# Performance work log

Measured on AMD Instinct MI355X. Metric: run time of the kernel, lower is better.

Reference implementation:

```python
import jax, jax.numpy as jnp
from jax import lax
import numpy as np
import math

V, D, N, L, KC, KL, B, S = 32000, 1024, 64, 4, 4, 4, 2, 1024
SCALE = 1.0 / math.sqrt(2 * L)   # base_layer.residual_scale
GAMMA = 0.01                     # lindblad_gamma
COND_TH = 100.0                  # condition_threshold
PHASE = np.complex64(np.exp(1j * 0.1))  # quaternionic escape rotation


def setup_inputs() -> dict:
    key = jax.random.key(0)
    ks = jax.random.split(key, 16)
    g = lambda k, shp, s=0.02: jax.random.normal(k, shp, jnp.float32) * s
    return {
        'token_ids': jax.random.randint(ks[0], (B, S), 0, V, dtype=jnp.int32),
        'emb_r': g(ks[1], (V, D)),
        'emb_i': g(ks[2], (V, D)),
        'W_in': g(ks[3], (L, D, 2 * D)),
        'conv_k': g(ks[4], (L, D, KC), 0.2),
        'A_log': jax.random.normal(ks[5], (L, D, N), jnp.float32) * 0.5,
        'dt_scale': g(ks[6], (L, D), 1.0),
        'dt_bias': jnp.full((L, D), -2.0, jnp.float32),
        'W_B': g(ks[7], (L, N, D)),
        'W_C': g(ks[8], (L, N, D)),
        'D_skip': g(ks[9], (L, D), 0.1),
        'W_out': g(ks[10], (L, D, D)),
        'L_ops': g(ks[11], (L, KL, D), 0.1),
        'norm_w': jnp.ones((D,), jnp.float32),
    }


def _dwconv(x, k):
    # causal depthwise conv; x [B,S,D] real, k [D,KC]
    xt = jnp.transpose(x, (0, 2, 1))  # [B,D,S]
    pad = k.shape[-1] - 1
    y = lax.conv_general_dilated(xt, k[:, None, :], (1,), [(pad, 0)],
                                 feature_group_count=k.shape[0])
    return jnp.transpose(y, (0, 2, 1))


def _csilu(x):
    # complex 'silu': x * sigmoid(|x|)
    return x * jax.nn.sigmoid(jnp.abs(x))


def _layer(x, Wi, ck, Alog, dts, dtb, WB, WC, Dk, Wo, Lops):
    residual = x
    xz = jnp.einsum('bsd,de->bse', x, Wi)          # complex [B,S,2D]
    x1, z = xz[..., :D], xz[..., D:]
    x1 = _dwconv(x1.real, ck) + 1j * _dwconv(x1.imag, ck)
    x1 = _csilu(x1)
    dt = jax.nn.softplus(x1.real * dts + dtb)      # [B,S,D] real
    A = -jnp.exp(Alog)                             # [D,N] real, stable
    Bc = jnp.einsum('bsd,nd->bsn', x1, WB)         # complex [B,S,N]
    Cc = jnp.einsum('bsd,nd->bsn', x1, WC)

    def step(h, inp):
        dt_t, x_t, B_t, C_t = inp                  # [B,D],[B,D],[B,N],[B,N]
        decay = jnp.exp(dt_t[..., None] * A)       # [B,D,N] real
        h = decay * h + (dt_t * x_t)[..., None] * B_t[:, None, :]
        y = jnp.einsum('bdn,bn->bd', h, C_t)
        return h, y

    h0 = jnp.zeros((x.shape[0], D, N), jnp.complex64)
    xs = (jnp.transpose(dt, (1, 0, 2)), jnp.transpose(x1, (1, 0, 2)),
          jnp.transpose(Bc, (1, 0, 2)), jnp.transpose(Cc, (1, 0, 2)))
    _, ys = lax.scan(step, h0, xs)                 # [S,B,D]
    y = jnp.transpose(ys, (1, 0, 2)) + Dk * x1
    y = y * _csilu(z)
    branch = jnp.einsum('bsd,de->bse', y, Wo)      # branch_out = (out-res)/scale

    # Lindblad dissipation: psi -> psi - gamma * sum_k L_k (L_k^H psi)
    proj = jnp.einsum('bsd,kd->bsk', branch, Lops)
    branch = branch - GAMMA * jnp.einsum('bsk,kd->bsd', proj, Lops)

    # H_eff = mean_s |psi_s><psi_s|; quaternionic escape uses its conditioning.
    # Only the diagonal is needed for the (diag-approx) condition number.
    diag = jnp.mean(jnp.abs(branch) ** 2, axis=1)  # [B,D]
    cond = jnp.max(diag, -1) / (jnp.min(diag, -1) + 1e-8)
    phase = jnp.where(cond > COND_TH, PHASE, jnp.complex64(1.0))  # [B]
    branch = branch * phase[:, None, None]

    # hybrid automata: _H_prev is None on first forward -> no jump (faithful)
    return residual + SCALE * branch


def reference(token_ids, emb_r, emb_i, W_in, conv_k, A_log, dt_scale, dt_bias,
              W_B, W_C, D_skip, W_out, L_ops, norm_w):
    psi = emb_r[token_ids] + 1j * emb_i[token_ids]   # [B,S,D] complex64
    for l in range(L):
        psi = _layer(psi, W_in[l], conv_k[l], A_log[l], dt_scale[l],
                     dt_bias[l], W_B[l], W_C[l], D_skip[l], W_out[l], L_ops[l])
    # ComplexRMSNorm
    rms = jnp.sqrt(jnp.mean(jnp.abs(psi) ** 2, -1, keepdims=True) + 1e-8)
    psi = psi / rms * norm_w
    # Born collapse sampler with weight tied to real embedding
    amp_r = jnp.einsum('bsd,vd->bsv', psi.real, emb_r)
    amp_i = jnp.einsum('bsd,vd->bsv', psi.imag, emb_r)
    logits = jnp.log(amp_r ** 2 + amp_i ** 2 + 1e-8)  # [B,S,V] real
    return logits
```

## Files before the change

kernel.cpp:

```cpp
#include <hip/hip_runtime.h>
#include <math.h>

#define BB 2
#define SS 1024
#define DD 1024
#define NN 64
#define LLAYERS 4
#define KCC 4
#define KLL 4
#define VV 32000
#define MM (BB*SS)
#define M2 (2*MM)
#define PS ((size_t)MM*DD)
#define CH 4
#define LC (SS/CH)
#define BDW (BB*DD)

#define SCALE_F 0.35355339059327373f
#define GAMMA_F 0.01f
#define PHASE_COS 0.99500416527802576f
#define PHASE_SIN 0.09983341664682815f

typedef _Float16 f16x8 __attribute__((ext_vector_type(8)));
typedef _Float16 f16x4 __attribute__((ext_vector_type(4)));
typedef float f32x4 __attribute__((ext_vector_type(4)));

__device__ __forceinline__ float softplus_f(float x) {
    return fmaxf(x, 0.f) + log1pf(expf(-fabsf(x)));
}

__device__ __forceinline__ void async16(void* lds_dst, const void* g_src) {
    __builtin_amdgcn_global_load_lds(
        (const __attribute__((address_space(1))) unsigned int*)g_src,
        (__attribute__((address_space(3))) unsigned int*)lds_dst,
        16, 0, 0);
}

__device__ __forceinline__ float rsum64_dpp(float v) {
    int x;
    x = __float_as_int(v);
    v += __int_as_float(__builtin_amdgcn_update_dpp(0, x, 0x111, 0xf, 0xf, true));
    x = __float_as_int(v);
    v += __int_as_float(__builtin_amdgcn_update_dpp(0, x, 0x112, 0xf, 0xf, true));
    x = __float_as_int(v);
    v += __int_as_float(__builtin_amdgcn_update_dpp(0, x, 0x114, 0xf, 0xf, true));
    x = __float_as_int(v);
    v += __int_as_float(__builtin_amdgcn_update_dpp(0, x, 0x118, 0xf, 0xf, true));
    x = __float_as_int(v);
    v += __int_as_float(__builtin_amdgcn_update_dpp(0, x, 0x142, 0xa, 0xf, true));
    x = __float_as_int(v);
    v += __int_as_float(__builtin_amdgcn_update_dpp(0, x, 0x143, 0xc, 0xf, true));
    return v;
}

__global__ __launch_bounds__(256) void k_split_w(const float* __restrict__ W,
        _Float16* __restrict__ Wh, _Float16* __restrict__ Wl, int Ksz, int Nsz) {
    __shared__ float t[32][33];
    int k0 = blockIdx.x * 32, n0 = blockIdx.y * 32;
    size_t base = (size_t)blockIdx.z * Ksz * Nsz;
    int r = threadIdx.x >> 3, c4 = (threadIdx.x & 7) * 4;
    float4 v = *(const float4*)(W + base + (size_t)(k0 + r) * Nsz + n0 + c4);
    t[r][c4 + 0] = v.x; t[r][c4 + 1] = v.y; t[r][c4 + 2] = v.z; t[r][c4 + 3] = v.w;
    __syncthreads();
    f16x4 hi, lo;
    #pragma unroll
    for (int j = 0; j < 4; ++j) {
        float x = t[c4 + j][r];
        _Float16 h = (_Float16)x;
        hi[j] = h; lo[j] = (_Float16)(x - (float)h);
    }
    size_t o = base + (size_t)(n0 + r) * Ksz + k0 + c4;
    *(f16x4*)(Wh + o) = hi;
    *(f16x4*)(Wl + o) = lo;
}

__global__ __launch_bounds__(256) void k_embed(const int* __restrict__ tok,
        const float* __restrict__ er, const float* __restrict__ ei,
        float* __restrict__ Pr, float* __restrict__ Pi,
        _Float16* __restrict__ Ph, _Float16* __restrict__ Pl) {
    int i = blockIdx.x * 256 + threadIdx.x;
    int d4 = (i & (DD/4 - 1)) * 4;
    int m  = i >> 8;
    int t = tok[m];
    float4 r  = *(const float4*)(er + (size_t)t * DD + d4);
    float4 im = *(const float4*)(ei + (size_t)t * DD + d4);
    size_t o = (size_t)m * DD + d4;
    *(float4*)(Pr + o) = r;
    *(float4*)(Pi + o) = im;
    float vr[4] = {r.x, r.y, r.z, r.w}, vi[4] = {im.x, im.y, im.z, im.w};
    f16x4 rh, rl, ih, il;
    #pragma unroll
    for (int j = 0; j < 4; ++j) {
        _Float16 h = (_Float16)vr[j]; rh[j] = h; rl[j] = (_Float16)(vr[j] - (float)h);
        _Float16 g = (_Float16)vi[j]; ih[j] = g; il[j] = (_Float16)(vi[j] - (float)g);
    }
    *(f16x4*)(Ph + o) = rh;      *(f16x4*)(Pl + o) = rl;
    *(f16x4*)(Ph + PS + o) = ih; *(f16x4*)(Pl + PS + o) = il;
}

__global__ __launch_bounds__(256, 2) void k_gemm_f16(
        const _Float16* __restrict__ Ah, const _Float16* __restrict__ Al,
        const _Float16* __restrict__ Bh, const _Float16* __restrict__ Bl,
        float* __restrict__ C, int Nsz) {
    __shared__ __align__(16) unsigned char lds[32768];
    const int lane = threadIdx.x & 63;
    const int wid  = threadIdx.x >> 6;
    const int wm = (wid >> 1) * 64;
    const int wv = (wid & 1) * 64;
    const int n0 = blockIdx.x * 128;
    const int m0 = blockIdx.y * 128;
    const int fr = lane & 15, fq = lane >> 4;

    f32x4 acc[4][4] = {};

    for (int k0 = 0; k0 < 1024; k0 += 32) {
        #pragma unroll
        for (int j = 0; j < 8; ++j) {
            int cid = wid * 8 + j;
            int sel = cid >> 3, c = cid & 7;
            const _Float16* bp = (sel == 0) ? Ah : (sel == 1) ? Al : (sel == 2) ? Bh : Bl;
            int rbase = ((sel < 2) ? m0 : n0) + c * 16 + fr;
            async16(lds + cid * 1024, bp + (size_t)rbase * 1024 + k0 + fq * 8);
        }
        __syncthreads();

        f16x8 ah[4], al[4];
        #pragma unroll
        for (int ms = 0; ms < 4; ++ms) {
            int off = ((wm >> 4) + ms) * 1024 + lane * 16;
            ah[ms] = *(const f16x8*)(lds + off);
            al[ms] = *(const f16x8*)(lds + 8192 + off);
        }
        #pragma unroll
        for (int vs = 0; vs < 4; ++vs) {
            int boff = ((wv >> 4) + vs) * 1024 + lane * 16;
            f16x8 bh = *(const f16x8*)(lds + 16384 + boff);
            f16x8 bl = *(const f16x8*)(lds + 24576 + boff);
            #pragma unroll
            for (int ms = 0; ms < 4; ++ms) {
                acc[ms][vs] = __builtin_amdgcn_mfma_f32_16x16x32_f16(ah[ms], bh, acc[ms][vs], 0, 0, 0);
                acc[ms][vs] = __builtin_amdgcn_mfma_f32_16x16x32_f16(ah[ms], bl, acc[ms][vs], 0, 0, 0);
                acc[ms][vs] = __builtin_amdgcn_mfma_f32_16x16x32_f16(al[ms], bh, acc[ms][vs], 0, 0, 0);
            }
        }
        __syncthreads();
    }

    #pragma unroll
    for (int ms = 0; ms < 4; ++ms) {
        #pragma unroll
        for (int vs = 0; vs < 4; ++vs) {
            #pragma unroll
            for (int r = 0; r < 4; ++r) {
                int row = m0 + wm + ms * 16 + fq * 4 + r;
                int col = n0 + wv + vs * 16 + fr;
                C[(size_t)row * Nsz + col] = acc[ms][vs][r];
            }
        }
    }
}

__global__ __launch_bounds__(256) void k_conv(const float* __restrict__ XZ,
        const float* __restrict__ ck, const float* __restrict__ dts,
        const float* __restrict__ dtb,
        float* __restrict__ Xr, float* __restrict__ Xi, float* __restrict__ DT,
        float* __restrict__ ZUr, float* __restrict__ ZUi) {
    int i = blockIdx.x * 256 + threadIdx.x;
    int d = i & (DD - 1);
    int m = i >> 10;
    int b = m >> 10, s = m & (SS - 1);
    float cr = 0.f, ci = 0.f;
    #pragma unroll
    for (int j = 0; j < KCC; ++j) {
        int sj = s - (KCC - 1) + j;
        if (sj >= 0) {
            int mm = (b << 10) + sj;
            float kw = ck[d * KCC + j];
            cr = fmaf(XZ[(size_t)mm * 2048 + d], kw, cr);
            ci = fmaf(XZ[(size_t)(MM + mm) * 2048 + d], kw, ci);
        }
    }
    float mag = sqrtf(cr*cr + ci*ci);
    float sg = 1.f / (1.f + expf(-mag));
    float xr = cr * sg, xi = ci * sg;
    Xr[i] = xr; Xi[i] = xi;
    DT[i] = softplus_f(fmaf(xr, dts[d], dtb[d]));
    float zr = XZ[(size_t)m * 2048 + DD + d];
    float zi = XZ[(size_t)(MM + m) * 2048 + DD + d];
    float mz = sqrtf(zr*zr + zi*zi);
    float sz = 1.f / (1.f + expf(-mz));
    ZUr[i] = zr * sz; ZUi[i] = zi * sz;
}

__global__ __launch_bounds__(256) void k_bc(const float* __restrict__ X,
        const float* __restrict__ WBp, const float* __restrict__ WCp,
        float* __restrict__ BC2) {
    __shared__ float xs[4][DD];
    __shared__ float red[4 * 256];
    int r0 = blockIdx.x * 4;
    for (int f = threadIdx.x; f < 4 * (DD / 4); f += 256) {
        int r = f / (DD / 4), c = (f % (DD / 4)) * 4;
        *(float4*)(&xs[r][c]) = *(const float4*)(X + (size_t)(r0 + r) * DD + c);
    }
    __syncthreads();
    int out = threadIdx.x & 127;
    int half = threadIdx.x >> 7;
    const float* Wrow = (out < 64) ? (WBp + (size_t)out * DD) : (WCp + (size_t)(out - 64) * DD);
    float acc[4] = {0.f, 0.f, 0.f, 0.f};
    for (int k = half * 512; k < half * 512 + 512; k += 4) {
        float4 w = *(const float4*)(Wrow + k);
        #pragma unroll
        for (int r = 0; r < 4; ++r) {
            float4 x4 = *(float4*)(&xs[r][k]);
            acc[r] = fmaf(x4.x, w.x, fmaf(x4.y, w.y, fmaf(x4.z, w.z, fmaf(x4.w, w.w, acc[r]))));
        }
    }
    #pragma unroll
    for (int r = 0; r < 4; ++r) red[r * 256 + threadIdx.x] = acc[r];
    __syncthreads();
    if (threadIdx.x < 128) {
        int isIm = (r0 >= MM) ? 1 : 0;
        int n = out & 63;
        int comp = ((out >> 6) << 1) | isIm;
        #pragma unroll
        for (int r = 0; r < 4; ++r) {
            float v = red[r * 256 + threadIdx.x] + red[r * 256 + threadIdx.x + 128];
            int m = (r0 + r) & (MM - 1);
            BC2[((size_t)m * 64 + n) * 4 + comp] = v;
        }
    }
}

__global__ __launch_bounds__(256, 8) void k_scan1(const float* __restrict__ X,
        const float* __restrict__ DT, const float4* __restrict__ BC2,
        const float* __restrict__ Alog, float* __restrict__ Y2,
        float2* __restrict__ HB, float* __restrict__ SDT) {
    int w = (blockIdx.x << 2) + (threadIdx.x >> 6);
    int lane = threadIdx.x & 63;
    int c = w & (CH - 1);
    int bd = w >> 2;
    int b = bd >> 10, d = bd & (DD - 1);
    float Av = -__expf(Alog[(size_t)d * NN + lane]);
    float hr = 0.f, hi = 0.f, sdt = 0.f;
    int s0 = c * LC, s1 = s0 + LC;
    size_t mBase = (size_t)(b << 10);
    size_t md = (mBase + s0) * DD + d;
    float dt_c = DT[md], xr_c = X[md], xi_c = X[PS + md];
    float4 bc_c = BC2[(mBase + s0) * 64 + lane];
    size_t mdc = md;
    for (int s = s0; s < s1; ++s) {
        int sn = (s + 1 < s1) ? (s + 1) : s;
        size_t mdn = (mBase + sn) * DD + d;
        float dt_n = DT[mdn], xr_n = X[mdn], xi_n = X[PS + mdn];
        float4 bc_n = BC2[(mBase + sn) * 64 + lane];
        float g = __expf(dt_c * Av);
        float dxr = dt_c * xr_c, dxi = dt_c * xi_c;
        hr = fmaf(g, hr, fmaf(dxr, bc_c.x, -dxi * bc_c.y));
        hi = fmaf(g, hi, fmaf(dxr, bc_c.y,  dxi * bc_c.x));
        sdt += dt_c;
        float yr = rsum64_dpp(hr * bc_c.z - hi * bc_c.w);
        float yi = rsum64_dpp(hr * bc_c.w + hi * bc_c.z);
        if (lane == 63) {
            Y2[mdc]      = yr;
            Y2[PS + mdc] = yi;
        }
        mdc += DD;
        dt_c = dt_n; xr_c = xr_n; xi_c = xi_n; bc_c = bc_n;
    }
    HB[((size_t)c * BDW + bd) * NN + lane] = make_float2(hr, hi);
    if (lane == 0) SDT[c * BDW + bd] = sdt;
}

__global__ __launch_bounds__(256, 8) void k_scan3(const float* __restrict__ DT,
        const float* __restrict__ BC2, const float* __restrict__ Alog,
        const float2* __restrict__ HB, const float* __restrict__ SDT,
        float* __restrict__ Y2) {
    int w = (blockIdx.x << 2) + (threadIdx.x >> 6);
    int lane = threadIdx.x & 63;
    int cm1 = w >> 11;
    int bd = w & (BDW - 1);
    int b = bd >> 10, d = bd & (DD - 1);
    float Av = -__expf(Alog[(size_t)d * NN + lane]);
    float2 h0 = HB[(size_t)bd * NN + lane];
    float hr = h0.x, hi = h0.y;
    if (cm1 >= 1) {
        float2 h1 = HB[((size_t)1 * BDW + bd) * NN + lane];
        float P1 = __expf(Av * SDT[1 * BDW + bd]);
        hr = fmaf(P1, hr, h1.x); hi = fmaf(P1, hi, h1.y);
        if (cm1 >= 2) {
            float2 h2 = HB[((size_t)2 * BDW + bd) * NN + lane];
            float P2 = __expf(Av * SDT[2 * BDW + bd]);
            hr = fmaf(P2, hr, h2.x); hi = fmaf(P2, hi, h2.y);
        }
    }
    int s0 = (cm1 + 1) * LC, s1 = s0 + LC;
    size_t mBase = (size_t)(b << 10);
    size_t md = (mBase + s0) * DD + d;
    float dt_c = DT[md];
    float2 cc_c = *(const float2*)(BC2 + ((mBase + s0) * 64 + lane) * 4 + 2);
    size_t mdc = md;
    for (int s = s0; s < s1; ++s) {
        int sn = (s + 1 < s1) ? (s + 1) : s;
        size_t mdn = (mBase + sn) * DD + d;
        float dt_n = DT[mdn];
        float2 cc_n = *(const float2*)(BC2 + ((mBase + sn) * 64 + lane) * 4 + 2);
        float g = __expf(dt_c * Av);
        hr *= g; hi *= g;
        float yr = rsum64_dpp(hr * cc_c.x - hi * cc_c.y);
        float yi = rsum64_dpp(hr * cc_c.y + hi * cc_c.x);
        if (lane == 63) {
            Y2[mdc]      += yr;
            Y2[PS + mdc] += yi;
        }
        mdc += DD;
        dt_c = dt_n; cc_c = cc_n;
    }
}

__global__ __launch_bounds__(256) void k_ymod(const float* __restrict__ Y2,
        const float* __restrict__ X, const float* __restrict__ ZUr,
        const float* __restrict__ ZUi, const float* __restrict__ Dk,
        _Float16* __restrict__ YOh, _Float16* __restrict__ YOl) {
    int i = blockIdx.x * 256 + threadIdx.x;
    int d = i & (DD - 1);
    float dk = Dk[d];
    float yr = Y2[i];
    float yi = Y2[PS + i];
    yr = fmaf(dk, X[i], yr);
    yi = fmaf(dk, X[PS + i], yi);
    float zr = ZUr[i], zi = ZUi[i];
    float or_ = yr * zr - yi * zi;
    float oi_ = yr * zi + yi * zr;
    _Float16 h0 = (_Float16)or_, h1 = (_Float16)oi_;
    YOh[i] = h0;      YOl[i] = (_Float16)(or_ - (float)h0);
    YOh[PS + i] = h1; YOl[PS + i] = (_Float16)(oi_ - (float)h1);
}

__global__ __launch_bounds__(256) void k_projcorr(float* __restrict__ BR,
        const float* __restrict__ Lop) {
    int row = (blockIdx.x << 2) + (threadIdx.x >> 6);
    int lane = threadIdx.x & 63;
    float* br = BR + (size_t)row * DD;
    float4 v[4], lw[4][4];
    float acc[4] = {0.f, 0.f, 0.f, 0.f};
    #pragma unroll
    for (int j = 0; j < 4; ++j) {
        int col = lane * 4 + j * 256;
        v[j] = *(const float4*)(br + col);
        #pragma unroll
        for (int k = 0; k < 4; ++k) {
            lw[j][k] = *(const float4*)(Lop + (size_t)k * DD + col);
            acc[k] += v[j].x * lw[j][k].x + v[j].y * lw[j][k].y
                    + v[j].z * lw[j][k].z + v[j].w * lw[j][k].w;
        }
    }
    #pragma unroll
    for (int off = 1; off <= 32; off <<= 1) {
        #pragma unroll
        for (int k = 0; k < 4; ++k) acc[k] += __shfl_xor(acc[k], off, 64);
    }
    #pragma unroll
    for (int j = 0; j < 4; ++j) {
        int col = lane * 4 + j * 256;
        float4 o;
        o.x = v[j].x - GAMMA_F * (acc[0]*lw[j][0].x + acc[1]*lw[j][1].x + acc[2]*lw[j][2].x + acc[3]*lw[j][3].x);
        o.y = v[j].y - GAMMA_F * (acc[0]*lw[j][0].y + acc[1]*lw[j][1].y + acc[2]*lw[j][2].y + acc[3]*lw[j][3].y);
        o.z = v[j].z - GAMMA_F * (acc[0]*lw[j][0].z + acc[1]*lw[j][1].z + acc[2]*lw[j][2].z + acc[3]*lw[j][3].z);
        o.w = v[j].w - GAMMA_F * (acc[0]*lw[j][0].w + acc[1]*lw[j][1].w + acc[2]*lw[j][2].w + acc[3]*lw[j][3].w);
        *(float4*)(br + col) = o;
    }
}

__global__ __launch_bounds__(256) void k_diag(const float* __restrict__ BR,
        float* __restrict__ DG) {
    __shared__ float red[4][64];
    int b = blockIdx.y, d0 = blockIdx.x * 64;
    int sg = threadIdx.x >> 6, ld = threadIdx.x & 63;
    float acc = 0.f;
    for (int s = sg; s < SS; s += 4) {
        size_t m = (size_t)(b * SS + s) * DD + d0 + ld;
        float r = BR[m], ii = BR[PS + m];
        acc = fmaf(r, r, fmaf(ii, ii, acc));
    }
    red[sg][ld] = acc;
    __syncthreads();
    if (threadIdx.x < 64) {
        float v = red[0][threadIdx.x] + red[1][threadIdx.x] + red[2][threadIdx.x] + red[3][threadIdx.x];
        DG[b * DD + d0 + threadIdx.x] = v * (1.f / SS);
    }
}

__global__ __launch_bounds__(256) void k_phase(const float* __restrict__ DG,
        float* __restrict__ PH) {
    __shared__ float mx[256], mn[256];
    int b = blockIdx.x;
    float vmax = -1e30f, vmin = 1e30f;
    for (int d = threadIdx.x; d < DD; d += 256) {
        float v = DG[b * DD + d];
        vmax = fmaxf(vmax, v); vmin = fminf(vmin, v);
    }
    mx[threadIdx.x] = vmax; mn[threadIdx.x] = vmin;
    __syncthreads();
    for (int st = 128; st >= 1; st >>= 1) {
        if (threadIdx.x < st) {
            mx[threadIdx.x] = fmaxf(mx[threadIdx.x], mx[threadIdx.x + st]);
            mn[threadIdx.x] = fminf(mn[threadIdx.x], mn[threadIdx.x + st]);
        }
        __syncthreads();
    }
    if (threadIdx.x == 0) {
        float cond = mx[0] / (mn[0] + 1e-8f);
        bool ap = cond > 100.0f;
        PH[b * 2 + 0] = ap ? PHASE_COS : 1.f;
        PH[b * 2 + 1] = ap ? PHASE_SIN : 0.f;
    }
}

__global__ __launch_bounds__(256) void k_resid(float* __restrict__ Pr,
        float* __restrict__ Pi, const float* __restrict__ BR,
        const float* __restrict__ PH,
        _Float16* __restrict__ Ph, _Float16* __restrict__ Pl) {
    int i = blockIdx.x * 256 + threadIdx.x;
    int b = i >> 20;
    float pr = PH[b * 2], pih = PH[b * 2 + 1];
    float brr = BR[i], bri = BR[PS + i];
    float nr = fmaf(SCALE_F, brr * pr - bri * pih, Pr[i]);
    float ni = fmaf(SCALE_F, brr * pih + bri * pr, Pi[i]);
    Pr[i] = nr; Pi[i] = ni;
    _Float16 h0 = (_Float16)nr, h1 = (_Float16)ni;
    Ph[i] = h0;      Pl[i] = (_Float16)(nr - (float)h0);
    Ph[PS + i] = h1; Pl[PS + i] = (_Float16)(ni - (float)h1);
}

__global__ __launch_bounds__(256) void k_rms(const float* __restrict__ Pr,
        const float* __restrict__ Pi, const float* __restrict__ nw,
        _Float16* __restrict__ Sp) {
    __shared__ float red[256];
    int m = blockIdx.x;
    int d = threadIdx.x * 4;
    float4 r  = *(const float4*)(Pr + (size_t)m * DD + d);
    float4 ii = *(const float4*)(Pi + (size_t)m * DD + d);
    float acc = r.x*r.x + r.y*r.y + r.z*r.z + r.w*r.w
              + ii.x*ii.x + ii.y*ii.y + ii.z*ii.z + ii.w*ii.w;
    red[threadIdx.x] = acc;
    __syncthreads();
    for (int st = 128; st >= 1; st >>= 1) {
        if (threadIdx.x < st) red[threadIdx.x] += red[threadIdx.x + st];
        __syncthreads();
    }
    float inv = 1.f / sqrtf(red[0] * (1.f / DD) + 1e-8f);
    float4 w = *(const float4*)(nw + d);
    float qr[4] = {r.x*inv*w.x, r.y*inv*w.y, r.z*inv*w.z, r.w*inv*w.w};
    float qi[4] = {ii.x*inv*w.x, ii.y*inv*w.y, ii.z*inv*w.z, ii.w*inv*w.w};
    f16x4 rh, rl, ih, il;
    #pragma unroll
    for (int j = 0; j < 4; ++j) {
        _Float16 h = (_Float16)qr[j]; rh[j] = h; rl[j] = (_Float16)(qr[j] - (float)h);
        _Float16 g = (_Float16)qi[j]; ih[j] = g; il[j] = (_Float16)(qi[j] - (float)g);
    }
    size_t o = (size_t)m * DD + d;
    *(f16x4*)(Sp + o)          = rh;
    *(f16x4*)(Sp + PS + o)     = rl;
    *(f16x4*)(Sp + 2 * PS + o) = ih;
    *(f16x4*)(Sp + 3 * PS + o) = il;
}

__global__ __launch_bounds__(256) void k_split_e(const float* __restrict__ E,
        _Float16* __restrict__ Eh, _Float16* __restrict__ El) {
    size_t i = (size_t)(blockIdx.x * 256 + threadIdx.x) * 8;
    float4 a = *(const float4*)(E + i);
    float4 b = *(const float4*)(E + i + 4);
    float v[8] = {a.x, a.y, a.z, a.w, b.x, b.y, b.z, b.w};
    f16x8 hi, lo;
    #pragma unroll
    for (int j = 0; j < 8; ++j) {
        _Float16 h = (_Float16)v[j];
        hi[j] = h; lo[j] = (_Float16)(v[j] - (float)h);
    }
    *(f16x8*)(Eh + i) = hi;
    *(f16x8*)(El + i) = lo;
}

__global__ __launch_bounds__(256, 2) void k_logits_mfma(
        const _Float16* __restrict__ Sp,
        const _Float16* __restrict__ Eh, const _Float16* __restrict__ El,
        float* __restrict__ out) {
    __shared__ __align__(16) unsigned char lds[49152];
    const int lane = threadIdx.x & 63;
    const int wid  = threadIdx.x >> 6;
    const int wm = (wid >> 1) * 64;
    const int wv = (wid & 1) * 64;
    const int fr = lane & 15, fq = lane >> 4;
    int x = blockIdx.x & 7;
    int j = blockIdx.x >> 3;
    const int m0 = ((x << 1) | (j & 1)) << 7;
    const int v0 = (j >> 1) << 7;

    f32x4 accR[4][4] = {};
    f32x4 accI[4][4] = {};

    for (int k0 = 0; k0 < DD; k0 += 32) {
        #pragma unroll
        for (int jj = 0; jj < 12; ++jj) {
            int cid = jj * 4 + wid;
            const _Float16* src;
            int ldsoff;
            if (cid < 32) {
                int p = cid >> 3, c = cid & 7;
                src = Sp + (size_t)p * PS + (size_t)(m0 + c * 16 + fr) * DD + k0 + fq * 8;
                ldsoff = p * 8192 + c * 1024;
            } else {
                int r = cid - 32;
                int q = r >> 3, c = r & 7;
                const _Float16* Ep = q ? El : Eh;
                src = Ep + (size_t)(v0 + c * 16 + fr) * DD + k0 + fq * 8;
                ldsoff = 32768 + q * 8192 + c * 1024;
            }
            async16(lds + ldsoff, src);
        }
        __syncthreads();

        f16x8 aRh[4], aRl[4], aIh[4], aIl[4];
        #pragma unroll
        for (int ms = 0; ms < 4; ++ms) {
            int off = ((wm >> 4) + ms) * 1024 + lane * 16;
            aRh[ms] = *(const f16x8*)(lds + off);
            aRl[ms] = *(const f16x8*)(lds + 8192 + off);
            aIh[ms] = *(const f16x8*)(lds + 16384 + off);
            aIl[ms] = *(const f16x8*)(lds + 24576 + off);
        }
        #pragma unroll
        for (int vs = 0; vs < 4; ++vs) {
            int boff = ((wv >> 4) + vs) * 1024 + lane * 16;
            f16x8 bh = *(const f16x8*)(lds + 32768 + boff);
            f16x8 bl = *(const f16x8*)(lds + 40960 + boff);
            #pragma unroll
            for (int ms = 0; ms < 4; ++ms) {
                accR[ms][vs] = __builtin_amdgcn_mfma_f32_16x16x32_f16(aRh[ms], bh, accR[ms][vs], 0, 0, 0);
                accR[ms][vs] = __builtin_amdgcn_mfma_f32_16x16x32_f16(aRh[ms], bl, accR[ms][vs], 0, 0, 0);
                accR[ms][vs] = __builtin_amdgcn_mfma_f32_16x16x32_f16(aRl[ms], bh, accR[ms][vs], 0, 0, 0);
                accI[ms][vs] = __builtin_amdgcn_mfma_f32_16x16x32_f16(aIh[ms], bh, accI[ms][vs], 0, 0, 0);
                accI[ms][vs] = __builtin_amdgcn_mfma_f32_16x16x32_f16(aIh[ms], bl, accI[ms][vs], 0, 0, 0);
                accI[ms][vs] = __builtin_amdgcn_mfma_f32_16x16x32_f16(aIl[ms], bh, accI[ms][vs], 0, 0, 0);
            }
        }
        __syncthreads();
    }

    #pragma unroll
    for (int ms = 0; ms < 4; ++ms) {
        #pragma unroll
        for (int vs = 0; vs < 4; ++vs) {
            #pragma unroll
            for (int r = 0; r < 4; ++r) {
                int row = m0 + wm + ms * 16 + fq * 4 + r;
                int col = v0 + wv + vs * 16 + fr;
                float ar = accR[ms][vs][r], ai = accI[ms][vs][r];
                out[(size_t)row * VV + col] = logf(fmaf(ar, ar, fmaf(ai, ai, 1e-8f)));
            }
        }
    }
}

extern "C" void kernel_launch(void* const* d_in, const int* in_sizes, int n_in,
                              void* d_out, int out_size, void* d_ws, size_t ws_size,
                              hipStream_t stream) {
    const int*   tok  = (const int*)d_in[0];
    const float* er   = (const float*)d_in[1];
    const float* ei   = (const float*)d_in[2];
    const float* Win  = (const float*)d_in[3];
    const float* ck   = (const float*)d_in[4];
    const float* Alog = (const float*)d_in[5];
    const float* dts  = (const float*)d_in[6];
    const float* dtb  = (const float*)d_in[7];
    const float* WB   = (const float*)d_in[8];
    const float* WC   = (const float*)d_in[9];
    const float* Dk   = (const float*)d_in[10];
    const float* Wo   = (const float*)d_in[11];
    const float* Lop  = (const float*)d_in[12];
    const float* nw   = (const float*)d_in[13];
    float* out = (float*)d_out;

    float* W0   = (float*)d_ws;
    float* P    = W0;
    float* XZ   = W0 + 2 * PS;
    float* X    = W0 + 6 * PS;
    float* DTp  = W0 + 8 * PS;
    float* ZU   = W0 + 9 * PS;
    float* Y2   = W0 + 11 * PS;
    _Float16* YOh = (_Float16*)(W0 + 19 * PS);
    _Float16* YOl = (_Float16*)(W0 + 20 * PS);
    _Float16* Ph  = (_Float16*)(W0 + 21 * PS);
    _Float16* Pl  = (_Float16*)(W0 + 22 * PS);
    float* BR   = XZ;
    float* BC2  = W0 + 23 * PS;
    float* DIAG = BC2 + (size_t)MM * 64 * 4;
    float* PH   = DIAG + BB * DD;
    float2* HB  = (float2*)(PH + 16);
    float* SDT  = (float*)(HB + (size_t)CH * BDW * NN);
    _Float16* Winh = (_Float16*)(W0 + 25 * PS);
    _Float16* Winl = (_Float16*)(W0 + 27 * PS);
    _Float16* Woh  = (_Float16*)(W0 + 29 * PS);
    _Float16* Wol  = (_Float16*)(W0 + 30 * PS);
    _Float16* Sp  = (_Float16*)(W0 + 2 * PS);
    _Float16* Ehp = (_Float16*)(W0 + 4 * PS);
    _Float16* Elp = (_Float16*)(W0 + 13 * PS);

    k_split_w<<<dim3(32, 64, 4), 256, 0, stream>>>(Win, Winh, Winl, 1024, 2048);
    k_split_w<<<dim3(32, 32, 4), 256, 0, stream>>>(Wo, Woh, Wol, 1024, 1024);

    k_embed<<<(int)(PS / 4 / 256), 256, 0, stream>>>(tok, er, ei, P, P + PS, Ph, Pl);

    for (int l = 0; l < LLAYERS; ++l) {
        const float* Lopl = Lop + (size_t)l * KLL * DD;
        const float* Alogl = Alog + (size_t)l * DD * NN;
        const _Float16* Wih = Winh + (size_t)l * 2048 * 1024;
        const _Float16* Wil = Winl + (size_t)l * 2048 * 1024;
        const _Float16* Wohl = Woh + (size_t)l * 1024 * 1024;
        const _Float16* Woll = Wol + (size_t)l * 1024 * 1024;

        k_gemm_f16<<<dim3(2048 / 128, M2 / 128), 256, 0, stream>>>(Ph, Pl, Wih, Wil, XZ, 2048);
        k_conv<<<(int)(MM * (size_t)DD / 256), 256, 0, stream>>>(XZ, ck + (size_t)l * DD * KCC,
                dts + l * DD, dtb + l * DD, X, X + PS, DTp, ZU, ZU + PS);
        k_bc<<<M2 / 4, 256, 0, stream>>>(X, WB + (size_t)l * NN * DD, WC + (size_t)l * NN * DD, BC2);
        k_scan1<<<(BDW * CH) / 4, 256, 0, stream>>>(X, DTp, (const float4*)BC2, Alogl, Y2, HB, SDT);
        k_scan3<<<(BDW * 3) / 4, 256, 0, stream>>>(DTp, BC2, Alogl, HB, SDT, Y2);
        k_ymod<<<(int)(MM * (size_t)DD / 256), 256, 0, stream>>>(Y2, X, ZU, ZU + PS, Dk + l * DD, YOh, YOl);
        k_gemm_f16<<<dim3(1024 / 128, M2 / 128), 256, 0, stream>>>(YOh, YOl, Wohl, Woll, BR, 1024);
        k_projcorr<<<M2 / 4, 256, 0, stream>>>(BR, Lopl);
        k_diag<<<dim3(DD / 64, BB), 256, 0, stream>>>(BR, DIAG);
        k_phase<<<BB, 256, 0, stream>>>(DIAG, PH);
        k_resid<<<(int)(PS / 256), 256, 0, stream>>>(P, P + PS, BR, PH, Ph, Pl);
    }

    k_rms<<<MM, 256, 0, stream>>>(P, P + PS, nw, Sp);
    k_split_e<<<(int)((size_t)VV * DD / 8 / 256), 256, 0, stream>>>(er, Ehp, Elp);
    k_logits_mfma<<<4000, 256, 0, stream>>>(Sp, Ehp, Elp, out);
}
```

Before: 3.683 ms.

## Store scan outputs in D-major layout and transpose through LDS in ymod

The scan kernels now write per-timestep outputs into a [b,d,s] transposed buffer, so consecutive steps of one wave land in consecutive addresses instead of strided by D. k_ymod becomes a 64x64 tiled kernel that reads the transposed tile with vector loads, transposes it in shared memory, then applies the skip and gate and the fp16 split in row-major order. The aim is to reduce the scattered single-lane stores and read-modify-writes in the scan loops, at the cost of an LDS transpose and a 2D launch in ymod.

```diff
diff --git a/kernel.cpp b/kernel.cpp
--- a/kernel.cpp
+++ b/kernel.cpp
@@ -233,7 +233,7 @@
 
 __global__ __launch_bounds__(256, 8) void k_scan1(const float* __restrict__ X,
         const float* __restrict__ DT, const float4* __restrict__ BC2,
-        const float* __restrict__ Alog, float* __restrict__ Y2,
+        const float* __restrict__ Alog, float* __restrict__ Y2T,
         float2* __restrict__ HB, float* __restrict__ SDT) {
     int w = (blockIdx.x << 2) + (threadIdx.x >> 6);
     int lane = threadIdx.x & 63;
@@ -247,7 +247,7 @@
     size_t md = (mBase + s0) * DD + d;
     float dt_c = DT[md], xr_c = X[md], xi_c = X[PS + md];
     float4 bc_c = BC2[(mBase + s0) * 64 + lane];
-    size_t mdc = md;
+    size_t ys = (size_t)bd * SS + s0;
     for (int s = s0; s < s1; ++s) {
         int sn = (s + 1 < s1) ? (s + 1) : s;
         size_t mdn = (mBase + sn) * DD + d;
@@ -261,10 +261,10 @@
         float yr = rsum64_dpp(hr * bc_c.z - hi * bc_c.w);
         float yi = rsum64_dpp(hr * bc_c.w + hi * bc_c.z);
         if (lane == 63) {
-            Y2[mdc]      = yr;
-            Y2[PS + mdc] = yi;
-        }
-        mdc += DD;
+            Y2T[ys]      = yr;
+            Y2T[PS + ys] = yi;
+        }
+        ++ys;
         dt_c = dt_n; xr_c = xr_n; xi_c = xi_n; bc_c = bc_n;
     }
     HB[((size_t)c * BDW + bd) * NN + lane] = make_float2(hr, hi);
@@ -274,7 +274,7 @@
 __global__ __launch_bounds__(256, 8) void k_scan3(const float* __restrict__ DT,
         const float* __restrict__ BC2, const float* __restrict__ Alog,
         const float2* __restrict__ HB, const float* __restrict__ SDT,
-        float* __restrict__ Y2) {
+        float* __restrict__ Y2T) {
     int w = (blockIdx.x << 2) + (threadIdx.x >> 6);
     int lane = threadIdx.x & 63;
     int cm1 = w >> 11;
@@ -298,7 +298,7 @@
     size_t md = (mBase + s0) * DD + d;
     float dt_c = DT[md];
     float2 cc_c = *(const float2*)(BC2 + ((mBase + s0) * 64 + lane) * 4 + 2);
-    size_t mdc = md;
+    size_t ys = (size_t)bd * SS + s0;
     for (int s = s0; s < s1; ++s) {
         int sn = (s + 1 < s1) ? (s + 1) : s;
         size_t mdn = (mBase + sn) * DD + d;
@@ -309,31 +309,51 @@
         float yr = rsum64_dpp(hr * cc_c.x - hi * cc_c.y);
         float yi = rsum64_dpp(hr * cc_c.y + hi * cc_c.x);
         if (lane == 63) {
-            Y2[mdc]      += yr;
-            Y2[PS + mdc] += yi;
-        }
-        mdc += DD;
+            Y2T[ys]      += yr;
+            Y2T[PS + ys] += yi;
+        }
+        ++ys;
         dt_c = dt_n; cc_c = cc_n;
     }
 }
 
-__global__ __launch_bounds__(256) void k_ymod(const float* __restrict__ Y2,
+__global__ __launch_bounds__(256) void k_ymod(const float* __restrict__ Y2T,
         const float* __restrict__ X, const float* __restrict__ ZUr,
         const float* __restrict__ ZUi, const float* __restrict__ Dk,
         _Float16* __restrict__ YOh, _Float16* __restrict__ YOl) {
-    int i = blockIdx.x * 256 + threadIdx.x;
-    int d = i & (DD - 1);
-    float dk = Dk[d];
-    float yr = Y2[i];
-    float yi = Y2[PS + i];
-    yr = fmaf(dk, X[i], yr);
-    yi = fmaf(dk, X[PS + i], yi);
-    float zr = ZUr[i], zi = ZUi[i];
-    float or_ = yr * zr - yi * zi;
-    float oi_ = yr * zi + yi * zr;
-    _Float16 h0 = (_Float16)or_, h1 = (_Float16)oi_;
-    YOh[i] = h0;      YOl[i] = (_Float16)(or_ - (float)h0);
-    YOh[PS + i] = h1; YOl[PS + i] = (_Float16)(oi_ - (float)h1);
+    __shared__ float tr[64][65];
+    __shared__ float ti[64][65];
+    int d0 = blockIdx.x * 64, m0 = blockIdx.y * 64;
+    int b = m0 >> 10, s0 = m0 & (SS - 1);
+    int t = threadIdx.x;
+    int rr = t >> 2, c0 = (t & 3) * 4;
+    size_t ybase = (size_t)(b * DD + d0 + rr) * SS + s0;
+    #pragma unroll
+    for (int j = 0; j < 4; ++j) {
+        float4 vr = *(const float4*)(Y2T + ybase + c0 + j * 16);
+        float4 vi = *(const float4*)(Y2T + PS + ybase + c0 + j * 16);
+        int sl = c0 + j * 16;
+        tr[sl + 0][rr] = vr.x; tr[sl + 1][rr] = vr.y; tr[sl + 2][rr] = vr.z; tr[sl + 3][rr] = vr.w;
+        ti[sl + 0][rr] = vi.x; ti[sl + 1][rr] = vi.y; ti[sl + 2][rr] = vi.z; ti[sl + 3][rr] = vi.w;
+    }
+    __syncthreads();
+    int td = t & 63, tq = t >> 6;
+    float dk = Dk[d0 + td];
+    #pragma unroll
+    for (int k = 0; k < 16; ++k) {
+        int tm = tq * 16 + k;
+        size_t i = (size_t)(m0 + tm) * DD + d0 + td;
+        float yr = tr[tm][td];
+        float yi = ti[tm][td];
+        yr = fmaf(dk, X[i], yr);
+        yi = fmaf(dk, X[PS + i], yi);
+        float zr = ZUr[i], zi = ZUi[i];
+        float or_ = yr * zr - yi * zi;
+        float oi_ = yr * zi + yi * zr;
+        _Float16 h0 = (_Float16)or_, h1 = (_Float16)oi_;
+        YOh[i] = h0;      YOl[i] = (_Float16)(or_ - (float)h0);
+        YOh[PS + i] = h1; YOl[PS + i] = (_Float16)(oi_ - (float)h1);
+    }
 }
 
 __global__ __launch_bounds__(256) void k_projcorr(float* __restrict__ BR,
@@ -587,7 +607,7 @@
     float* X    = W0 + 6 * PS;
     float* DTp  = W0 + 8 * PS;
     float* ZU   = W0 + 9 * PS;
-    float* Y2   = W0 + 11 * PS;
+    float* Y2T  = W0 + 11 * PS;
     _Float16* YOh = (_Float16*)(W0 + 19 * PS);
     _Float16* YOl = (_Float16*)(W0 + 20 * PS);
     _Float16* Ph  = (_Float16*)(W0 + 21 * PS);
@@ -623,9 +643,9 @@
         k_conv<<<(int)(MM * (size_t)DD / 256), 256, 0, stream>>>(XZ, ck + (size_t)l * DD * KCC,
                 dts + l * DD, dtb + l * DD, X, X + PS, DTp, ZU, ZU + PS);
         k_bc<<<M2 / 4, 256, 0, stream>>>(X, WB + (size_t)l * NN * DD, WC + (size_t)l * NN * DD, BC2);
-        k_scan1<<<(BDW * CH) / 4, 256, 0, stream>>>(X, DTp, (const float4*)BC2, Alogl, Y2, HB, SDT);
-        k_scan3<<<(BDW * 3) / 4, 256, 0, stream>>>(DTp, BC2, Alogl, HB, SDT, Y2);
-        k_ymod<<<(int)(MM * (size_t)DD / 256), 256, 0, stream>>>(Y2, X, ZU, ZU + PS, Dk + l * DD, YOh, YOl);
+        k_scan1<<<(BDW * CH) / 4, 256, 0, stream>>>(X, DTp, (const float4*)BC2, Alogl, Y2T, HB, SDT);
+        k_scan3<<<(BDW * 3) / 4, 256, 0, stream>>>(DTp, BC2, Alogl, HB, SDT, Y2T);
+        k_ymod<<<dim3(DD / 64, MM / 64), 256, 0, stream>>>(Y2T, X, ZU, ZU + PS, Dk + l * DD, YOh, YOl);
         k_gemm_f16<<<dim3(1024 / 128, M2 / 128), 256, 0, stream>>>(YOh, YOl, Wohl, Woll, BR, 1024);
         k_projcorr<<<M2 / 4, 256, 0, stream>>>(BR, Lopl);
         k_diag<<<dim3(DD / 64, BB), 256, 0, stream>>>(BR, DIAG);
```

Result: no change. 3.636 ms (-1.3%).
